# Performance work log

Measured on AMD Instinct MI355X. Metric: run time of the kernel, lower is better.

Reference implementation:

```python
import jax, jax.numpy as jnp
import numpy as np

A = -0.75  # torch bicubic cubic-convolution coefficient

def _cubic_weights(t):
    # t in [0,1); returns 4 tap weights matching torch's upsample_get_cubic_coefficients
    def cc1(x):  # |x| <= 1
        return ((A + 2.0) * x - (A + 3.0)) * x * x + 1.0
    def cc2(x):  # 1 < |x| < 2
        return ((A * x - 5.0 * A) * x + 8.0 * A) * x - 4.0 * A
    return jnp.stack([cc2(t + 1.0), cc1(t), cc1(1.0 - t), cc2(2.0 - t)], axis=-1)  # (N,4)

def _axis_taps(coord, size):
    # align_corners=True unnormalization, border padding = clamp tap indices
    ix = (coord + 1.0) * 0.5 * (size - 1)
    x0 = jnp.floor(ix)
    w = _cubic_weights(ix - x0)                                   # (N,4)
    idx = jnp.clip(x0.astype(jnp.int32)[:, None] + jnp.arange(-1, 3), 0, size - 1)  # (N,4)
    return w, idx

def _sample_plane(plane, coords):
    # plane (C,H,W); coords (N,2) with x->W, y->H; bicubic, border, align_corners=True
    C, H, W = plane.shape
    wx, xi = _axis_taps(coords[:, 0], W)
    wy, yi = _axis_taps(coords[:, 1], H)
    out = jnp.zeros((C, coords.shape[0]), plane.dtype)
    for i in range(4):
        for j in range(4):
            out = out + (wy[:, i] * wx[:, j])[None, :] * plane[:, yi[:, i], xi[:, j]]
    return out.T  # (N,C)

def _sample_vector(vec, coord):
    # vec (C,G); width dim of the (C,G,1) vector collapses to tap 0 with weight 1
    wy, yi = _axis_taps(coord, vec.shape[1])
    out = jnp.zeros((vec.shape[0], coord.shape[0]), vec.dtype)
    for i in range(4):
        out = out + wy[:, i][None, :] * vec[:, yi[:, i]]
    return out.T  # (N,C)

def _triplane(planes, coords):
    # planes (3,C,H,W); coords (N,3); xy, yz, xz projections
    return (_sample_plane(planes[0], coords[:, 0:2])
            + _sample_plane(planes[1], coords[:, 1:3])
            + _sample_plane(planes[2], coords[:, ::2]))

def setup_inputs() -> dict:
    key = jax.random.key(0)
    k0, k1, k2, k3, k4 = jax.random.split(key, 5)
    N, C, G = 524288, 32, 512
    coordinates = jax.random.uniform(k0, (N, 3), jnp.float32, minval=-1.0, maxval=1.0)
    plane3 = jax.random.normal(k1, (3, C, G // 4, G // 4), jnp.float32) * 0.00015
    plane2 = jax.random.normal(k2, (3, C, G // 2, G // 2), jnp.float32) * 0.0003
    vec1 = jax.random.normal(k3, (3, C, G), jnp.float32) * 0.001
    B = jax.random.normal(k4, (4 * C, 2 * C), jnp.float32) * 0.0075
    return {"coordinates": coordinates, "plane3": plane3, "plane2": plane2, "vec1": vec1, "B": B}

def reference(coordinates, plane3, plane2, vec1, B):
    f3 = _triplane(plane3, coordinates)            # feature1 == feature2 in the original
    f2 = _triplane(plane2, coordinates)
    fv = (_sample_vector(vec1[0], coordinates[:, 0])
          + _sample_vector(vec1[1], coordinates[:, 1])
          + _sample_vector(vec1[2], coordinates[:, 2]))
    feat = jnp.concatenate([f3, f3, f2, fv], axis=-1)  # (N, 4C)
    proj = (feat @ B) * jnp.asarray(2.0 * np.pi, feat.dtype)
    return jnp.concatenate([jnp.sin(proj), jnp.cos(proj)], axis=-1)  # (N, 4C)
```

## Files before the change

kernel.cpp:

```cpp
#include <hip/hip_runtime.h>
#include <hip/hip_bf16.h>
#include <stdint.h>

typedef float f32x2 __attribute__((ext_vector_type(2)));
typedef float f32x4 __attribute__((ext_vector_type(4)));
typedef short s16x8 __attribute__((ext_vector_type(8)));

#define CUBIC_A (-0.75f)
#define S3 262144.0f
#define S2 131072.0f
#define SV 32768.0f

#define PL3 (128 * 132 * 32)
#define PL2 (256 * 260 * 32)
#define PLV (516 * 32)
#define STRIDE3 (132 * 32)
#define STRIDE2 (260 * 32)

#define NBINS 32768

__device__ __forceinline__ void cubic_w(float t, float* w) {
  float s = t + 1.0f;
  w[0] = ((CUBIC_A * s - 5.0f * CUBIC_A) * s + 8.0f * CUBIC_A) * s - 4.0f * CUBIC_A;
  w[1] = ((CUBIC_A + 2.0f) * t - (CUBIC_A + 3.0f)) * t * t + 1.0f;
  float u = 1.0f - t;
  w[2] = ((CUBIC_A + 2.0f) * u - (CUBIC_A + 3.0f)) * u * u + 1.0f;
  float v = 2.0f - t;
  w[3] = ((CUBIC_A * v - 5.0f * CUBIC_A) * v + 8.0f * CUBIC_A) * v - 4.0f * CUBIC_A;
}

__device__ __forceinline__ void axis_w(float c, int size, float* w, int* colb) {
  float ix = (c + 1.0f) * 0.5f * (float)(size - 1);
  float x0f = floorf(ix);
  cubic_w(ix - x0f, w);
  *colb = (int)x0f * 32;
}

__device__ __forceinline__ void axis_r(float c, int size, int strideB, float* w, int* ro) {
  float ix = (c + 1.0f) * 0.5f * (float)(size - 1);
  float x0f = floorf(ix);
  cubic_w(ix - x0f, w);
  int x0 = (int)x0f;
#pragma unroll
  for (int k = 0; k < 4; ++k) {
    int qq = x0 - 1 + k;
    qq = qq < 0 ? 0 : qq;
    qq = qq > size - 1 ? size - 1 : qq;
    ro[k] = qq * strideB;
  }
}

__device__ __forceinline__ void axis_wr(float c, int size, int strideB, float* w, int* colb, int* ro) {
  float ix = (c + 1.0f) * 0.5f * (float)(size - 1);
  float x0f = floorf(ix);
  cubic_w(ix - x0f, w);
  int x0 = (int)x0f;
  *colb = x0 * 32;
#pragma unroll
  for (int k = 0; k < 4; ++k) {
    int qq = x0 - 1 + k;
    qq = qq < 0 ? 0 : qq;
    qq = qq > size - 1 ? size - 1 : qq;
    ro[k] = qq * strideB;
  }
}

__device__ __forceinline__ void issueW(const uint8_t* __restrict__ base,
                                       const int* ro, int cb, uint4* r) {
#pragma unroll
  for (int i = 0; i < 4; ++i) {
    r[2 * i]     = *reinterpret_cast<const uint4*>(base + ro[i] + cb);
    r[2 * i + 1] = *reinterpret_cast<const uint4*>(base + ro[i] + cb + 64);
  }
}

__device__ __forceinline__ void consume16(uint4 v, float w, f32x2* acc8) {
  f32x2 w2; w2.x = w; w2.y = w;
  acc8[0] += w2 * __builtin_amdgcn_cvt_pk_f32_fp8((int)v.x, false);
  acc8[1] += w2 * __builtin_amdgcn_cvt_pk_f32_fp8((int)v.x, true);
  acc8[2] += w2 * __builtin_amdgcn_cvt_pk_f32_fp8((int)v.y, false);
  acc8[3] += w2 * __builtin_amdgcn_cvt_pk_f32_fp8((int)v.y, true);
  acc8[4] += w2 * __builtin_amdgcn_cvt_pk_f32_fp8((int)v.z, false);
  acc8[5] += w2 * __builtin_amdgcn_cvt_pk_f32_fp8((int)v.z, true);
  acc8[6] += w2 * __builtin_amdgcn_cvt_pk_f32_fp8((int)v.w, false);
  acc8[7] += w2 * __builtin_amdgcn_cvt_pk_f32_fp8((int)v.w, true);
}

__device__ __forceinline__ void consumeW(const float* wr, float cw0, float cw1,
                                         const uint4* r, f32x2* acc8) {
#pragma unroll
  for (int i = 0; i < 4; ++i) {
    consume16(r[2 * i],     wr[i] * cw0, acc8);
    consume16(r[2 * i + 1], wr[i] * cw1, acc8);
  }
}


__device__ __forceinline__ int bin_of(float x, float y, float z) {
  int bx = (int)((x + 1.0f) * 16.0f); bx = bx < 0 ? 0 : (bx > 31 ? 31 : bx);
  int by = (int)((y + 1.0f) * 16.0f); by = by < 0 ? 0 : (by > 31 ? 31 : by);
  int bz = (int)((z + 1.0f) * 16.0f); bz = bz < 0 ? 0 : (bz > 31 ? 31 : bz);
  return (bz << 10) | (by << 5) | bx;
}

__global__ void __launch_bounds__(256) zero_hist(uint32_t* __restrict__ hist) {
  int i = blockIdx.x * 256 + threadIdx.x;
  if (i < NBINS) hist[i] = 0;
}

__global__ void __launch_bounds__(256) hist_kernel(const float* __restrict__ coords,
                                                   uint32_t* __restrict__ hist, int N) {
  int i = blockIdx.x * 256 + threadIdx.x;
  if (i >= N) return;
  int b = bin_of(coords[3 * i], coords[3 * i + 1], coords[3 * i + 2]);
  atomicAdd(&hist[b], 1u);
}

__global__ void __launch_bounds__(1024) scan_kernel(const uint32_t* __restrict__ hist,
                                                    uint32_t* __restrict__ offs) {
  __shared__ uint32_t s[1024];
  int t = threadIdx.x;
  uint32_t sum = 0;
#pragma unroll
  for (int k = 0; k < 32; ++k) sum += hist[t * 32 + k];
  s[t] = sum;
  __syncthreads();
  for (int d = 1; d < 1024; d <<= 1) {
    uint32_t v = (t >= d) ? s[t - d] : 0;
    __syncthreads();
    s[t] += v;
    __syncthreads();
  }
  uint32_t run = (t == 0) ? 0 : s[t - 1];
#pragma unroll
  for (int k = 0; k < 32; ++k) {
    offs[t * 32 + k] = run;
    run += hist[t * 32 + k];
  }
}

__global__ void __launch_bounds__(256) scatter_kernel(const float* __restrict__ coords,
                                                      uint32_t* __restrict__ offs,
                                                      float4* __restrict__ sorted, int N) {
  int i = blockIdx.x * 256 + threadIdx.x;
  if (i >= N) return;
  float x = coords[3 * i], y = coords[3 * i + 1], z = coords[3 * i + 2];
  int b = bin_of(x, y, z);
  uint32_t pos = atomicAdd(&offs[b], 1u);
  float4 v; v.x = x; v.y = y; v.z = z; v.w = __int_as_float(i);
  sorted[pos] = v;
}


__device__ __forceinline__ float comb_row(const float* __restrict__ B, int r, int j) {
  return (r < 32) ? (B[r * 64 + j] + B[(r + 32) * 64 + j]) : B[(r + 32) * 64 + j];
}

__device__ __forceinline__ uint32_t pack_bf16(float v0, float v1) {
  uint32_t a = __float_as_uint(v0);
  uint32_t b = __float_as_uint(v1);
  uint32_t r0 = (a + 0x7fffu + ((a >> 16) & 1u)) >> 16;
  uint32_t r1 = (b + 0x7fffu + ((b >> 16) & 1u)) >> 16;
  return (r0 & 0xffffu) | (r1 << 16);
}

__global__ void __launch_bounds__(256) make_bfrag(const float* __restrict__ B, uint4* __restrict__ Bf) {
  int i = blockIdx.x * 256 + threadIdx.x;
  if (i >= 768) return;
  int lane = i & 63;
  int cb = (i >> 6) & 3;
  int seg = i >> 8;
  float invS = (seg == 0) ? (1.0f / S3) : (seg == 1) ? (1.0f / S2) : (1.0f / SV);
  int j = cb * 16 + (lane & 15);
  int h = lane >> 4;
  uint32_t o[4];
#pragma unroll
  for (int r = 0; r < 4; ++r) {
    int k0 = seg * 32 + h * 8 + 2 * r;
    float v0 = comb_row(B, k0, j) * invS;
    float v1 = comb_row(B, k0 + 1, j) * invS;
    o[r] = pack_bf16(v0, v1);
  }
  uint4 st; st.x = o[0]; st.y = o[1]; st.z = o[2]; st.w = o[3];
  Bf[(seg * 4 + cb) * 64 + lane] = st;
}

__global__ void __launch_bounds__(256) transpose_cl8(const float* __restrict__ in,
                                                     uint8_t* __restrict__ out,
                                                     int H, int W, int Wp, int nxt, float S) {
  __shared__ float tile[32][65];
  int b = blockIdx.x;
  int xt = b % nxt;
  int tmp = b / nxt;
  int y = tmp % H;
  int p = tmp / H;
  int x0 = xt * 64;
  int lane = threadIdx.x;
  const float* src = in + ((size_t)p * 32 * (size_t)H) * (size_t)W + (size_t)y * (size_t)W;
  int cx = lane & 63;
  int c4 = lane >> 6;
#pragma unroll
  for (int pass = 0; pass < 8; ++pass) {
    int c = pass * 4 + c4;
    tile[c][cx] = src[(size_t)c * (size_t)(H) * (size_t)W + x0 + cx];
  }
  __syncthreads();
  int xx = lane >> 2;
  int c8 = (lane & 3) * 8;
  float f[8];
#pragma unroll
  for (int i = 0; i < 8; ++i) f[i] = tile[c8 + i][xx] * S;
  uint32_t lo = 0, hi = 0;
  lo = (uint32_t)__builtin_amdgcn_cvt_pk_fp8_f32(f[0], f[1], (int)lo, false);
  lo = (uint32_t)__builtin_amdgcn_cvt_pk_fp8_f32(f[2], f[3], (int)lo, true);
  hi = (uint32_t)__builtin_amdgcn_cvt_pk_fp8_f32(f[4], f[5], (int)hi, false);
  hi = (uint32_t)__builtin_amdgcn_cvt_pk_fp8_f32(f[6], f[7], (int)hi, true);
  uint2 st; st.x = lo; st.y = hi;
  int x = x0 + xx;
  uint8_t* rowb = out + (((size_t)p * H + y) * (size_t)Wp) * 32;
  *reinterpret_cast<uint2*>(rowb + (size_t)(x + 1) * 32 + c8) = st;
  if (x == 0)
    *reinterpret_cast<uint2*>(rowb + c8) = st;
  if (x == W - 1) {
    *reinterpret_cast<uint2*>(rowb + (size_t)(W + 1) * 32 + c8) = st;
    *reinterpret_cast<uint2*>(rowb + (size_t)(W + 2) * 32 + c8) = st;
  }
}


__global__ void __launch_bounds__(256, 4) triplane_main(
    const float4* __restrict__ sorted,
    const uint8_t* __restrict__ p3t,
    const uint8_t* __restrict__ p2t,
    const uint8_t* __restrict__ vt,
    const uint4* __restrict__ Bfrag,
    float* __restrict__ out, int N) {
  int t = blockIdx.x * 256 + threadIdx.x;
  int l = threadIdx.x & 63;
  int n0 = (blockIdx.x * 256 + (threadIdx.x & ~63)) >> 2;
  if (n0 >= N) return;
  int n = t >> 2;
  int q = l & 3;
  bool hiq = (q >> 1) != 0;
  int q16 = q * 16;

  float4 pd = sorted[n];
  float x = pd.x;
  float y = pd.y;
  float z = pd.z;
  int oidx = __float_as_int(pd.w);

  f32x2 feat2[24];
#pragma unroll
  for (int i = 0; i < 24; ++i) { feat2[i].x = 0.f; feat2[i].y = 0.f; }

  uint4 rA[8], rB[8];

  float wx[4], wy[4], wz[4];
  int cbx, cby, roy[4], roz[4];
  axis_w(x, 128, wx, &cbx);
  axis_wr(y, 128, STRIDE3, wy, &cby, roy);
  axis_r(z, 128, STRIDE3, wz, roz);
  float cx0 = hiq ? wx[1] : wx[0], cx1 = hiq ? wx[3] : wx[2];
  float cy0 = hiq ? wy[1] : wy[0], cy1 = hiq ? wy[3] : wy[2];

  const uint8_t* b3 = p3t + q16;
  issueW(b3,           roy, cbx, rA);
  issueW(b3 + 1 * PL3, roz, cby, rB);
  consumeW(wy, cx0, cx1, rA, feat2 + 0);
  issueW(b3 + 2 * PL3, roz, cbx, rA);
  consumeW(wz, cy0, cy1, rB, feat2 + 0);

  float wx2[4], wy2[4], wz2[4];
  int cbx2, cby2, roy2[4], roz2[4];
  axis_w(x, 256, wx2, &cbx2);
  axis_wr(y, 256, STRIDE2, wy2, &cby2, roy2);
  axis_r(z, 256, STRIDE2, wz2, roz2);
  float cx20 = hiq ? wx2[1] : wx2[0], cx21 = hiq ? wx2[3] : wx2[2];
  float cy20 = hiq ? wy2[1] : wy2[0], cy21 = hiq ? wy2[3] : wy2[2];

  const uint8_t* b2 = p2t + q16;
  issueW(b2,           roy2, cbx2, rB);
  consumeW(wz, cx0, cx1, rA, feat2 + 0);
  issueW(b2 + 1 * PL2, roz2, cby2, rA);
  consumeW(wy2, cx20, cx21, rB, feat2 + 8);
  issueW(b2 + 2 * PL2, roz2, cbx2, rB);
  consumeW(wz2, cy20, cy21, rA, feat2 + 8);

  float wvx[4], wvy[4], wvz[4];
  int cbvx, cbvy, cbvz;
  axis_w(x, 512, wvx, &cbvx);
  axis_w(y, 512, wvy, &cbvy);
  axis_w(z, 512, wvz, &cbvz);
  {
    const uint8_t* v0 = vt + q16;
    rA[0] = *reinterpret_cast<const uint4*>(v0 + cbvx);
    rA[1] = *reinterpret_cast<const uint4*>(v0 + cbvx + 64);
    rA[2] = *reinterpret_cast<const uint4*>(v0 + PLV + cbvy);
    rA[3] = *reinterpret_cast<const uint4*>(v0 + PLV + cbvy + 64);
    rA[4] = *reinterpret_cast<const uint4*>(v0 + 2 * PLV + cbvz);
    rA[5] = *reinterpret_cast<const uint4*>(v0 + 2 * PLV + cbvz + 64);
  }
  consumeW(wz2, cx20, cx21, rB, feat2 + 8);
  {
    float a0 = hiq ? wvx[1] : wvx[0], a1 = hiq ? wvx[3] : wvx[2];
    float b0 = hiq ? wvy[1] : wvy[0], b1 = hiq ? wvy[3] : wvy[2];
    float c0 = hiq ? wvz[1] : wvz[0], c1 = hiq ? wvz[3] : wvz[2];
    consume16(rA[0], a0, feat2 + 16);
    consume16(rA[1], a1, feat2 + 16);
    consume16(rA[2], b0, feat2 + 16);
    consume16(rA[3], b1, feat2 + 16);
    consume16(rA[4], c0, feat2 + 16);
    consume16(rA[5], c1, feat2 + 16);
  }

  uint32_t packed[12];
#pragma unroll
  for (int s = 0; s < 3; ++s) {
#pragma unroll
    for (int r = 0; r < 4; ++r) {
      f32x2 lo = feat2[s * 8 + r];
      f32x2 hi = feat2[s * 8 + 4 + r];
      float ownx = hiq ? hi.x : lo.x, owny = hiq ? hi.y : lo.y;
      float sndx = hiq ? lo.x : hi.x, sndy = hiq ? lo.y : hi.y;
      float rx = ownx + __shfl_xor(sndx, 2);
      float ry = owny + __shfl_xor(sndy, 2);
      uint32_t pk;
      asm("v_cvt_pk_bf16_f32 %0, %1, %2" : "=v"(pk) : "v"(rx), "v"(ry));
      packed[s * 4 + r] = pk;
    }
  }

  int hp = l >> 4;
  int srcq = ((hp & 1) << 1) | (hp >> 1);
  int baddr = (4 * (l & 15) + srcq) * 4;
  uint32_t apk[12];
#pragma unroll
  for (int i = 0; i < 12; ++i)
    apk[i] = (uint32_t)__builtin_amdgcn_ds_bpermute(baddr, (int)packed[i]);

  int rowr[4];
#pragma unroll
  for (int reg = 0; reg < 4; ++reg)
    rowr[reg] = __shfl(oidx, 16 * hp + 4 * reg);

  uint4 bfr[12];
#pragma unroll
  for (int i = 0; i < 12; ++i) bfr[i] = Bfrag[i * 64 + l];

  union U { uint32_t u[4]; s16x8 v; };
  f32x4 acc[4];
#pragma unroll
  for (int cb = 0; cb < 4; ++cb) { acc[cb].x = 0.f; acc[cb].y = 0.f; acc[cb].z = 0.f; acc[cb].w = 0.f; }
#pragma unroll
  for (int seg = 0; seg < 3; ++seg) {
    U a;
    a.u[0] = apk[seg * 4 + 0];
    a.u[1] = apk[seg * 4 + 1];
    a.u[2] = apk[seg * 4 + 2];
    a.u[3] = apk[seg * 4 + 3];
#pragma unroll
    for (int cb = 0; cb < 4; ++cb) {
      U b;
      b.u[0] = bfr[seg * 4 + cb].x;
      b.u[1] = bfr[seg * 4 + cb].y;
      b.u[2] = bfr[seg * 4 + cb].z;
      b.u[3] = bfr[seg * 4 + cb].w;
      acc[cb] = __builtin_amdgcn_mfma_f32_16x16x32_bf16(a.v, b.v, acc[cb], 0, 0, 0);
    }
  }

  int jc = l & 15;
#pragma unroll
  for (int cb = 0; cb < 4; ++cb) {
#pragma unroll
    for (int reg = 0; reg < 4; ++reg) {
      float v = acc[cb][reg];
      float sv = __builtin_amdgcn_sinf(v);
      float cv = __builtin_amdgcn_cosf(v);
      float* po = out + (size_t)rowr[reg] * 128 + cb * 16 + jc;
      po[0] = sv;
      po[64] = cv;
    }
  }
}


extern "C" void kernel_launch(void* const* d_in, const int* in_sizes, int n_in,
                              void* d_out, int out_size, void* d_ws, size_t ws_size,
                              hipStream_t stream) {
  const float* coords = (const float*)d_in[0];
  const float* plane3 = (const float*)d_in[1];
  const float* plane2 = (const float*)d_in[2];
  const float* vec1   = (const float*)d_in[3];
  const float* B      = (const float*)d_in[4];
  float* out = (float*)d_out;
  int N = in_sizes[0] / 3;

  char* ws = (char*)d_ws;
  size_t off = 0;
  auto take = [&](size_t bytes) { size_t o = off; off = (off + bytes + 4095) & ~(size_t)4095; return o; };
  const size_t off_p3 = take((size_t)3 * PL3);
  const size_t off_p2 = take((size_t)3 * PL2);
  const size_t off_vt = take((size_t)3 * PLV);
  const size_t off_bf = take(768 * 16);
  const size_t off_hist = take(NBINS * 4);
  const size_t off_offs = take(NBINS * 4);
  const size_t off_sorted = take((size_t)N * 16);
  uint8_t* p3t = (uint8_t*)(ws + off_p3);
  uint8_t* p2t = (uint8_t*)(ws + off_p2);
  uint8_t* vt  = (uint8_t*)(ws + off_vt);
  uint4* Bf = (uint4*)(ws + off_bf);
  uint32_t* hist = (uint32_t*)(ws + off_hist);
  uint32_t* offs = (uint32_t*)(ws + off_offs);
  float4* sorted = (float4*)(ws + off_sorted);

  hipLaunchKernelGGL(make_bfrag, dim3(3), dim3(256), 0, stream, B, Bf);
  hipLaunchKernelGGL(transpose_cl8, dim3(3 * 128 * 2), dim3(256), 0, stream, plane3, p3t, 128, 128, 132, 2, S3);
  hipLaunchKernelGGL(transpose_cl8, dim3(3 * 256 * 4), dim3(256), 0, stream, plane2, p2t, 256, 256, 260, 4, S2);
  hipLaunchKernelGGL(transpose_cl8, dim3(3 * 1 * 8), dim3(256), 0, stream, vec1, vt, 1, 512, 516, 8, SV);
  hipLaunchKernelGGL(zero_hist, dim3(NBINS / 256), dim3(256), 0, stream, hist);
  hipLaunchKernelGGL(hist_kernel, dim3((N + 255) / 256), dim3(256), 0, stream, coords, hist, N);
  hipLaunchKernelGGL(scan_kernel, dim3(1), dim3(1024), 0, stream, hist, offs);
  hipLaunchKernelGGL(scatter_kernel, dim3((N + 255) / 256), dim3(256), 0, stream, coords, offs, sorted, N);
  hipLaunchKernelGGL(triplane_main, dim3((N * 4 + 255) / 256), dim3(256), 0, stream,
                     sorted, p3t, p2t, vt, Bf, out, N);
}
```

Measured before the change: 196.6 us.

## Merge prep kernels into one launch and raise main kernel occupancy bound

```diff
diff --git a/kernel.cpp b/kernel.cpp
--- a/kernel.cpp
+++ b/kernel.cpp
@@ -103,54 +103,6 @@
   return (bz << 10) | (by << 5) | bx;
 }
 
-__global__ void __launch_bounds__(256) zero_hist(uint32_t* __restrict__ hist) {
-  int i = blockIdx.x * 256 + threadIdx.x;
-  if (i < NBINS) hist[i] = 0;
-}
-
-__global__ void __launch_bounds__(256) hist_kernel(const float* __restrict__ coords,
-                                                   uint32_t* __restrict__ hist, int N) {
-  int i = blockIdx.x * 256 + threadIdx.x;
-  if (i >= N) return;
-  int b = bin_of(coords[3 * i], coords[3 * i + 1], coords[3 * i + 2]);
-  atomicAdd(&hist[b], 1u);
-}
-
-__global__ void __launch_bounds__(1024) scan_kernel(const uint32_t* __restrict__ hist,
-                                                    uint32_t* __restrict__ offs) {
-  __shared__ uint32_t s[1024];
-  int t = threadIdx.x;
-  uint32_t sum = 0;
-#pragma unroll
-  for (int k = 0; k < 32; ++k) sum += hist[t * 32 + k];
-  s[t] = sum;
-  __syncthreads();
-  for (int d = 1; d < 1024; d <<= 1) {
-    uint32_t v = (t >= d) ? s[t - d] : 0;
-    __syncthreads();
-    s[t] += v;
-    __syncthreads();
-  }
-  uint32_t run = (t == 0) ? 0 : s[t - 1];
-#pragma unroll
-  for (int k = 0; k < 32; ++k) {
-    offs[t * 32 + k] = run;
-    run += hist[t * 32 + k];
-  }
-}
-
-__global__ void __launch_bounds__(256) scatter_kernel(const float* __restrict__ coords,
-                                                      uint32_t* __restrict__ offs,
-                                                      float4* __restrict__ sorted, int N) {
-  int i = blockIdx.x * 256 + threadIdx.x;
-  if (i >= N) return;
-  float x = coords[3 * i], y = coords[3 * i + 1], z = coords[3 * i + 2];
-  int b = bin_of(x, y, z);
-  uint32_t pos = atomicAdd(&offs[b], 1u);
-  float4 v; v.x = x; v.y = y; v.z = z; v.w = __int_as_float(i);
-  sorted[pos] = v;
-}
-
 
 __device__ __forceinline__ float comb_row(const float* __restrict__ B, int r, int j) {
   return (r < 32) ? (B[r * 64 + j] + B[(r + 32) * 64 + j]) : B[(r + 32) * 64 + j];
@@ -164,8 +116,7 @@
   return (r0 & 0xffffu) | (r1 << 16);
 }
 
-__global__ void __launch_bounds__(256) make_bfrag(const float* __restrict__ B, uint4* __restrict__ Bf) {
-  int i = blockIdx.x * 256 + threadIdx.x;
+__device__ __forceinline__ void bfrag_body(int i, const float* __restrict__ B, uint4* __restrict__ Bf) {
   if (i >= 768) return;
   int lane = i & 63;
   int cb = (i >> 6) & 3;
@@ -185,11 +136,10 @@
   Bf[(seg * 4 + cb) * 64 + lane] = st;
 }
 
-__global__ void __launch_bounds__(256) transpose_cl8(const float* __restrict__ in,
-                                                     uint8_t* __restrict__ out,
-                                                     int H, int W, int Wp, int nxt, float S) {
+__device__ __forceinline__ void transpose_body(int b, const float* __restrict__ in,
+                                               uint8_t* __restrict__ out,
+                                               int H, int W, int Wp, int nxt, float S) {
   __shared__ float tile[32][65];
-  int b = blockIdx.x;
   int xt = b % nxt;
   int tmp = b / nxt;
   int y = tmp % H;
@@ -227,8 +177,73 @@
   }
 }
 
-
-__global__ void __launch_bounds__(256, 4) triplane_main(
+#define PREP_BLOCKS 3995
+__global__ void __launch_bounds__(256) prep_all(const float* __restrict__ B, uint4* __restrict__ Bf,
+                                                uint32_t* __restrict__ hist,
+                                                const float* __restrict__ plane3, uint8_t* __restrict__ p3t,
+                                                const float* __restrict__ plane2, uint8_t* __restrict__ p2t,
+                                                const float* __restrict__ vec1, uint8_t* __restrict__ vt) {
+  int bid = blockIdx.x;
+  if (bid < 3) {
+    bfrag_body(bid * 256 + threadIdx.x, B, Bf);
+  } else if (bid < 131) {
+    int i = (bid - 3) * 256 + threadIdx.x;
+    if (i < NBINS) hist[i] = 0;
+  } else if (bid < 899) {
+    transpose_body(bid - 131, plane3, p3t, 128, 128, 132, 2, S3);
+  } else if (bid < 3971) {
+    transpose_body(bid - 899, plane2, p2t, 256, 256, 260, 4, S2);
+  } else {
+    transpose_body(bid - 3971, vec1, vt, 1, 512, 516, 8, SV);
+  }
+}
+
+
+__global__ void __launch_bounds__(256) hist_kernel(const float* __restrict__ coords,
+                                                   uint32_t* __restrict__ hist, int N) {
+  int i = blockIdx.x * 256 + threadIdx.x;
+  if (i >= N) return;
+  int b = bin_of(coords[3 * i], coords[3 * i + 1], coords[3 * i + 2]);
+  atomicAdd(&hist[b], 1u);
+}
+
+__global__ void __launch_bounds__(1024) scan_kernel(const uint32_t* __restrict__ hist,
+                                                    uint32_t* __restrict__ offs) {
+  __shared__ uint32_t s[1024];
+  int t = threadIdx.x;
+  uint32_t sum = 0;
+#pragma unroll
+  for (int k = 0; k < 32; ++k) sum += hist[t * 32 + k];
+  s[t] = sum;
+  __syncthreads();
+  for (int d = 1; d < 1024; d <<= 1) {
+    uint32_t v = (t >= d) ? s[t - d] : 0;
+    __syncthreads();
+    s[t] += v;
+    __syncthreads();
+  }
+  uint32_t run = (t == 0) ? 0 : s[t - 1];
+#pragma unroll
+  for (int k = 0; k < 32; ++k) {
+    offs[t * 32 + k] = run;
+    run += hist[t * 32 + k];
+  }
+}
+
+__global__ void __launch_bounds__(256) scatter_kernel(const float* __restrict__ coords,
+                                                      uint32_t* __restrict__ offs,
+                                                      float4* __restrict__ sorted, int N) {
+  int i = blockIdx.x * 256 + threadIdx.x;
+  if (i >= N) return;
+  float x = coords[3 * i], y = coords[3 * i + 1], z = coords[3 * i + 2];
+  int b = bin_of(x, y, z);
+  uint32_t pos = atomicAdd(&offs[b], 1u);
+  float4 v; v.x = x; v.y = y; v.z = z; v.w = __int_as_float(i);
+  sorted[pos] = v;
+}
+
+
+__global__ void __launch_bounds__(256, 6) triplane_main(
     const float4* __restrict__ sorted,
     const uint8_t* __restrict__ p3t,
     const uint8_t* __restrict__ p2t,
@@ -415,11 +430,8 @@
   uint32_t* offs = (uint32_t*)(ws + off_offs);
   float4* sorted = (float4*)(ws + off_sorted);
 
-  hipLaunchKernelGGL(make_bfrag, dim3(3), dim3(256), 0, stream, B, Bf);
-  hipLaunchKernelGGL(transpose_cl8, dim3(3 * 128 * 2), dim3(256), 0, stream, plane3, p3t, 128, 128, 132, 2, S3);
-  hipLaunchKernelGGL(transpose_cl8, dim3(3 * 256 * 4), dim3(256), 0, stream, plane2, p2t, 256, 256, 260, 4, S2);
-  hipLaunchKernelGGL(transpose_cl8, dim3(3 * 1 * 8), dim3(256), 0, stream, vec1, vt, 1, 512, 516, 8, SV);
-  hipLaunchKernelGGL(zero_hist, dim3(NBINS / 256), dim3(256), 0, stream, hist);
+  hipLaunchKernelGGL(prep_all, dim3(PREP_BLOCKS), dim3(256), 0, stream,
+                     B, Bf, hist, plane3, p3t, plane2, p2t, vec1, vt);
   hipLaunchKernelGGL(hist_kernel, dim3((N + 255) / 256), dim3(256), 0, stream, coords, hist, N);
   hipLaunchKernelGGL(scan_kernel, dim3(1), dim3(1024), 0, stream, hist, offs);
   hipLaunchKernelGGL(scatter_kernel, dim3((N + 255) / 256), dim3(256), 0, stream, coords, offs, sorted, N);
```

Measured after the change: 186.4 us. -5.2%, faster.
